# Kernel optimization log

Measured on AMD Instinct MI355X. Metric: run time of the kernel, lower is better.

The kernel has to match this reference:

```python
import jax, jax.numpy as jnp
import numpy as np

B, C, H, W = 8, 512, 64, 64
KD, VD, OD = 64, 512, 512
BN_EPS = 1e-5


def setup_inputs() -> dict:
    key = jax.random.key(0)
    ks = jax.random.split(key, 10)
    s = lambda fan_in: 1.0 / np.sqrt(fan_in)
    return {
        "x": jax.random.normal(ks[0], (B, C, H, W), jnp.float32),
        "Wq": jax.random.normal(ks[1], (KD, C), jnp.float32) * s(C),
        "bq": jnp.zeros((KD,), jnp.float32),
        "Wk": jax.random.normal(ks[2], (KD, C), jnp.float32) * s(C),
        "bk": jnp.zeros((KD,), jnp.float32),
        "Wv": jax.random.normal(ks[3], (VD, C), jnp.float32) * s(C),
        "bv": jnp.zeros((VD,), jnp.float32),
        "gamma": jnp.zeros((1,), jnp.float32),  # torch init: zeros(1)
        "Wf": jax.random.normal(ks[4], (OD, VD), jnp.float32) * s(VD),
        "bn_w": jnp.ones((OD,), jnp.float32),
        "bn_b": jnp.zeros((OD,), jnp.float32),
        "bn_mean": jnp.zeros((OD,), jnp.float32),
        "bn_var": jnp.ones((OD,), jnp.float32),
    }


def reference(x, Wq, bq, Wk, bk, Wv, bv, gamma, Wf, bn_w, bn_b, bn_mean, bn_var):
    b, c, h, w = x.shape
    n = h * w
    # 1x1 convs == per-pixel channel matmuls
    q = jnp.einsum('bchw,kc->bkhw', x, Wq) + bq[None, :, None, None]  # [B,KD,H,W]
    k = jnp.einsum('bchw,kc->bkhw', x, Wk) + bk[None, :, None, None]
    v = jnp.einsum('bchw,vc->bvhw', x, Wv) + bv[None, :, None, None]
    q = q.reshape(b, -1, n)  # [B,KD,N]
    k = k.reshape(b, -1, n)
    v = v.reshape(b, -1, n)  # [B,VD,N]
    # energy[b, i, j] = q[:, :, i] . k[:, :, j]   (proj_query permuted)
    energy = jnp.einsum('bki,bkj->bij', q, k)  # [B,N,N]
    attention = jax.nn.softmax(energy, axis=-1)
    # out = value @ attention^T : out[b, v, i] = sum_j value[b, v, j] * attention[b, i, j]
    out = jnp.einsum('bvj,bij->bvi', v, attention)  # [B,VD,N]
    out = out.reshape(b, c, h, w)
    out = gamma * out + x
    # fuse: 1x1 conv (no bias) -> BatchNorm (inference) -> ReLU
    fused = jnp.einsum('bchw,oc->bohw', out, Wf)
    inv = jax.lax.rsqrt(bn_var + BN_EPS)
    fused = (fused - bn_mean[None, :, None, None]) * (bn_w * inv)[None, :, None, None] + bn_b[None, :, None, None]
    return jax.nn.relu(fused)
```

## Files before the change

### kernel.cpp

```cpp
#include <hip/hip_runtime.h>
#include <hip/hip_bf16.h>

typedef unsigned short u16;
typedef unsigned int u32;
typedef __attribute__((ext_vector_type(8))) short bf16x8;
typedef __attribute__((ext_vector_type(4))) float f32x4;
typedef __attribute__((ext_vector_type(4))) u16 u16x4;

#define B_ 8
#define C_ 512
#define N_ 4096
#define KD_ 64
#define VD_ 512
#define OD_ 512

static __device__ __forceinline__ float bf2f(u16 u) {
    union { u32 i; float f; } z; z.i = ((u32)u) << 16; return z.f;
}
static __device__ __forceinline__ u16 f2bf(float f) {
    union { float f; u32 u; } v; v.f = f;
    u32 r = v.u + 0x7fffu + ((v.u >> 16) & 1u);
    return (u16)(r >> 16);
}
static __device__ __forceinline__ u32 pkbf(float lo, float hi) {
    u32 ul = __float_as_uint(lo) + 0x8000u;
    u32 uh = __float_as_uint(hi) + 0x8000u;
    return __builtin_amdgcn_perm(uh, ul, 0x07060302u);
}
static __device__ __forceinline__ int swz(int row) { return ((row >> 2) + (row >> 4)) & 3; }

static __device__ __forceinline__ void tile_barrier() {
    asm volatile("s_waitcnt lgkmcnt(0)" ::: "memory");
    __builtin_amdgcn_s_barrier();
    asm volatile("" ::: "memory");
}

__global__ __launch_bounds__(256) void transpose_convert_kernel(
    const float* __restrict__ x, const float* __restrict__ Wf,
    const float* __restrict__ gamma,
    u16* __restrict__ xT, u16* __restrict__ Wf16)
{
    const int t = threadIdx.x;
    if (blockIdx.x >= 256) {
        const int tid = (blockIdx.x - 256) * 256 + t;
        const float4* src = (const float4*)Wf + (size_t)tid * 16;
        u16* dst = Wf16 + (size_t)tid * 64;
        #pragma unroll
        for (int j = 0; j < 16; j++) {
            const float4 f = src[j];
            u16x4 p;
            p[0] = f2bf(f.x); p[1] = f2bf(f.y); p[2] = f2bf(f.z); p[3] = f2bf(f.w);
            *(u16x4*)(dst + j * 4) = p;
        }
        return;
    }
    if (gamma[0] == 0.0f) return;
    __shared__ u32 tile[64][33];
    for (int it = 0; it < 16; it++) {
        const int bid = it * 256 + blockIdx.x;
        const int nt = bid & 63;
        const int ct = (bid >> 6) & 7;
        const int b  = bid >> 9;
        const float* xb  = x  + ((size_t)b * C_ + ct * 64) * N_ + nt * 64;
        u16*         xTb = xT + ((size_t)b * N_ + nt * 64) * C_ + ct * 64;
        {
            const int p  = t >> 3;
            const int n8 = t & 7;
            const float* r0 = xb + (size_t)(2 * p)     * N_ + n8 * 8;
            const float* r1 = xb + (size_t)(2 * p + 1) * N_ + n8 * 8;
            const float4 a0 = *(const float4*)(r0);
            const float4 a1 = *(const float4*)(r0 + 4);
            const float4 c0 = *(const float4*)(r1);
            const float4 c1 = *(const float4*)(r1 + 4);
            const float av[8] = { a0.x, a0.y, a0.z, a0.w, a1.x, a1.y, a1.z, a1.w };
            const float cv[8] = { c0.x, c0.y, c0.z, c0.w, c1.x, c1.y, c1.z, c1.w };
            #pragma unroll
            for (int j = 0; j < 8; j++)
                tile[n8 * 8 + j][p] = (u32)f2bf(av[j]) | ((u32)f2bf(cv[j]) << 16);
        }
        __syncthreads();
        #pragma unroll
        for (int h = 0; h < 2; h++) {
            const int id = t + h * 256;
            const int n  = id >> 3;
            const int q  = id & 7;
            uint4 val;
            val.x = tile[n][q * 4 + 0];
            val.y = tile[n][q * 4 + 1];
            val.z = tile[n][q * 4 + 2];
            val.w = tile[n][q * 4 + 3];
            *(uint4*)(xTb + (size_t)n * C_ + q * 8) = val;
        }
        __syncthreads();
    }
}

__global__ __launch_bounds__(256) void proj_kernel(
    const u16* __restrict__ xT,
    const float* __restrict__ Wq, const float* __restrict__ bq,
    const float* __restrict__ Wk, const float* __restrict__ bk,
    const float* __restrict__ Wv, const float* __restrict__ bv,
    const float* __restrict__ gamma,
    u16* __restrict__ q, u16* __restrict__ k, u16* __restrict__ v)
{
    if (gamma[0] == 0.0f) return;
    for (int it = 0; it < 2; it++) {
        const int bid = it * 256 + blockIdx.x;
        const int b = bid >> 6;
        const int p = (bid & 63) * 64 + (threadIdx.x & 63);
        const int dg = threadIdx.x >> 6;
        const u16* xrow = xT + ((size_t)b * N_ + p) * C_;
        for (int d0 = dg * 160; d0 < dg * 160 + 160; d0++) {
            const float* wrow; float bias; u16* dst; int dd; int dim;
            if (d0 < 64)       { dd = d0;       wrow = Wq + (size_t)dd * C_; bias = bq[dd]; dst = q; dim = KD_; }
            else if (d0 < 128) { dd = d0 - 64;  wrow = Wk + (size_t)dd * C_; bias = bk[dd]; dst = k; dim = KD_; }
            else               { dd = d0 - 128; wrow = Wv + (size_t)dd * C_; bias = bv[dd]; dst = v; dim = VD_; }
            float s = bias;
            for (int c = 0; c < C_; c++) s += bf2f(xrow[c]) * wrow[c];
            dst[((size_t)b * dim + dd) * N_ + p] = f2bf(s);
        }
    }
}

__global__ __launch_bounds__(256) void attn_kernel(
    const u16* __restrict__ xT, const u16* __restrict__ q,
    const u16* __restrict__ k, const u16* __restrict__ v,
    const float* __restrict__ gamma, u16* __restrict__ yT)
{
    const float g = gamma[0];
    if (g == 0.0f) return;
    __shared__ float pls[4][64];
    const int wv = threadIdx.x >> 6, lane = threadIdx.x & 63;
    for (int it = 0; it < 4; it++) {
        const int bid = it * 256 + blockIdx.x;
        const int b  = bid >> 7;
        const int q0 = (bid & 127) * 32 + wv * 8;
        const u16* kb = k + (size_t)b * KD_ * N_;
        const u16* vb = v + (size_t)b * VD_ * N_;
        for (int qi = 0; qi < 8; qi++) {
            const int i = q0 + qi;
            const float qv = bf2f(q[((size_t)b * KD_ + lane) * N_ + i]);
            float mx = -1e30f, l = 0.f;
            for (int jb = 0; jb < N_; jb += 64) {
                float e = 0.f;
                for (int kd = 0; kd < 64; kd++)
                    e += __shfl(qv, kd) * bf2f(kb[(size_t)kd * N_ + jb + lane]);
                const float nm = fmaxf(mx, e);
                l = l * __expf(mx - nm) + __expf(e - nm);
                mx = nm;
            }
            for (int off = 32; off; off >>= 1) {
                const float mo = __shfl_xor(mx, off);
                const float lo = __shfl_xor(l, off);
                const float nm = fmaxf(mx, mo);
                l = l * __expf(mx - nm) + lo * __expf(mo - nm);
                mx = nm;
            }
            float oacc[8];
            #pragma unroll
            for (int r = 0; r < 8; r++) oacc[r] = 0.f;
            for (int jb = 0; jb < N_; jb += 64) {
                float e = 0.f;
                for (int kd = 0; kd < 64; kd++)
                    e += __shfl(qv, kd) * bf2f(kb[(size_t)kd * N_ + jb + lane]);
                __syncthreads();
                pls[wv][lane] = __expf(e - mx);
                __syncthreads();
                for (int jj = 0; jj < 64; jj++) {
                    const float p = pls[wv][jj];
                    #pragma unroll
                    for (int r = 0; r < 8; r++)
                        oacc[r] += p * bf2f(vb[(size_t)(r * 64 + lane) * N_ + jb + jj]);
                }
            }
            const float inv = 1.f / l;
            #pragma unroll
            for (int r = 0; r < 8; r++) {
                const size_t idx = ((size_t)b * N_ + i) * C_ + r * 64 + lane;
                yT[idx] = f2bf(g * oacc[r] * inv + bf2f(xT[idx]));
            }
        }
    }
}

__global__ __launch_bounds__(256, 3) void gemm_bn_relu(
    const float* __restrict__ x, const u16* __restrict__ yT,
    const u16* __restrict__ Wf16, const float* __restrict__ gamma,
    const float* __restrict__ bnw, const float* __restrict__ bnb,
    const float* __restrict__ bnm, const float* __restrict__ bnv,
    float* __restrict__ out)
{
    __shared__ u16 lds_x[2][128 * 32];
    __shared__ u16 lds_w[2][128 * 32];

    const int bid = blockIdx.x;
    const int pt8 = bid & 7;
    const int ot  = (bid >> 3) & 3;
    const int g   = bid >> 5;
    const int pt  = (g & 3) * 8 + pt8;
    const int b   = g >> 2;

    const int t = threadIdx.x;
    const int lane = t & 63;
    const int wv = t >> 6;
    const int wm = wv >> 1;
    const int wn = wv & 1;
    const int lcol = lane & 15;
    const int kq = lane >> 4;

    const int rw = t >> 2, posw = t & 3;
    const int ql = (posw - swz(rw)) & 3;
    const u16* WT0 = Wf16 + (size_t)(ot * 128 + rw) * C_ + ql * 8;
    const u16* WT1 = WT0 + (size_t)64 * C_;
    const int wla0 = rw * 32 + posw * 8;
    const int wla1 = wla0 + 64 * 32;

    int aaddr[4], baddr[4];
    #pragma unroll
    for (int i = 0; i < 4; i++) {
        const int P = wm * 64 + i * 16 + lcol;
        aaddr[i] = P * 32 + ((kq + swz(P)) & 3) * 8;
        const int R = wn * 64 + i * 16 + lcol;
        baddr[i] = R * 32 + ((kq + swz(R)) & 3) * 8;
    }

    f32x4 acc[4][4];
    #pragma unroll
    for (int i = 0; i < 4; i++)
        #pragma unroll
        for (int j = 0; j < 4; j++)
            acc[i][j] = (f32x4){0.f, 0.f, 0.f, 0.f};

    auto compute = [&](int buf) {
        bf16x8 af[4], bfg[4];
        #pragma unroll
        for (int mi = 0; mi < 4; mi++)
            af[mi] = *(const bf16x8*)&lds_x[buf][aaddr[mi]];
        #pragma unroll
        for (int ni = 0; ni < 4; ni++)
            bfg[ni] = *(const bf16x8*)&lds_w[buf][baddr[ni]];
        #pragma unroll
        for (int mi = 0; mi < 4; mi++)
            #pragma unroll
            for (int ni = 0; ni < 4; ni++)
                acc[mi][ni] = __builtin_amdgcn_mfma_f32_16x16x32_bf16(
                    af[mi], bfg[ni], acc[mi][ni], 0, 0, 0);
    };

    if (gamma[0] == 0.0f) {
        const int q4 = t & 15, cp = t >> 4;
        int xidx[8];
        #pragma unroll
        for (int j = 0; j < 8; j++) {
            const int p = q4 + 16 * j;
            xidx[j] = p * 16 + (((cp >> 2) + swz(p)) & 3) * 4 + (cp & 3);
        }
        const float* eptr = x + ((size_t)b * C_ + 2 * cp) * N_ + pt * 128 + q4;
        const float* optr = eptr + N_;

        float eA_[8], oA_[8], eB_[8], oB_[8];
        uint4 wA0, wA1, wB0, wB1;
        auto loadA = [&](int ks) {
            const float* ee = eptr + (size_t)ks * 32 * N_;
            const float* oo = optr + (size_t)ks * 32 * N_;
            #pragma unroll
            for (int j = 0; j < 8; j++) { eA_[j] = ee[16 * j]; oA_[j] = oo[16 * j]; }
            wA0 = *(const uint4*)(WT0 + ks * 32);
            wA1 = *(const uint4*)(WT1 + ks * 32);
        };
        auto loadB = [&](int ks) {
            const float* ee = eptr + (size_t)ks * 32 * N_;
            const float* oo = optr + (size_t)ks * 32 * N_;
            #pragma unroll
            for (int j = 0; j < 8; j++) { eB_[j] = ee[16 * j]; oB_[j] = oo[16 * j]; }
            wB0 = *(const uint4*)(WT0 + ks * 32);
            wB1 = *(const uint4*)(WT1 + ks * 32);
        };
        auto writeA = [&](int buf) {
            u32* lx = (u32*)lds_x[buf];
            #pragma unroll
            for (int j = 0; j < 8; j++) lx[xidx[j]] = pkbf(eA_[j], oA_[j]);
            *(uint4*)&lds_w[buf][wla0] = wA0;
            *(uint4*)&lds_w[buf][wla1] = wA1;
        };
        auto writeB = [&](int buf) {
            u32* lx = (u32*)lds_x[buf];
            #pragma unroll
            for (int j = 0; j < 8; j++) lx[xidx[j]] = pkbf(eB_[j], oB_[j]);
            *(uint4*)&lds_w[buf][wla0] = wB0;
            *(uint4*)&lds_w[buf][wla1] = wB1;
        };

        loadA(0); loadB(1);
        writeA(0);
        for (int ks = 0; ks < 16; ks += 2) {
            tile_barrier();
            if (ks + 2 < 16) loadA(ks + 2);
            compute(0);
            writeB(1);
            tile_barrier();
            if (ks + 3 < 16) loadB(ks + 3);
            compute(1);
            if (ks + 2 < 16) writeA(0);
        }
    } else {
        const u16* YT0 = yT + ((size_t)b * N_ + pt * 128 + rw) * C_ + ql * 8;
        const u16* YT1 = YT0 + (size_t)64 * C_;
        uint4 yA0, yA1, yB0, yB1, wA0, wA1, wB0, wB1;
        auto loadA = [&](int ks) {
            yA0 = *(const uint4*)(YT0 + ks * 32);
            yA1 = *(const uint4*)(YT1 + ks * 32);
            wA0 = *(const uint4*)(WT0 + ks * 32);
            wA1 = *(const uint4*)(WT1 + ks * 32);
        };
        auto loadB = [&](int ks) {
            yB0 = *(const uint4*)(YT0 + ks * 32);
            yB1 = *(const uint4*)(YT1 + ks * 32);
            wB0 = *(const uint4*)(WT0 + ks * 32);
            wB1 = *(const uint4*)(WT1 + ks * 32);
        };
        auto writeA = [&](int buf) {
            *(uint4*)&lds_x[buf][wla0] = yA0;
            *(uint4*)&lds_x[buf][wla1] = yA1;
            *(uint4*)&lds_w[buf][wla0] = wA0;
            *(uint4*)&lds_w[buf][wla1] = wA1;
        };
        auto writeB = [&](int buf) {
            *(uint4*)&lds_x[buf][wla0] = yB0;
            *(uint4*)&lds_x[buf][wla1] = yB1;
            *(uint4*)&lds_w[buf][wla0] = wB0;
            *(uint4*)&lds_w[buf][wla1] = wB1;
        };

        loadA(0); loadB(1);
        writeA(0);
        for (int ks = 0; ks < 16; ks += 2) {
            tile_barrier();
            if (ks + 2 < 16) loadA(ks + 2);
            compute(0);
            writeB(1);
            tile_barrier();
            if (ks + 3 < 16) loadB(ks + 3);
            compute(1);
            if (ks + 2 < 16) writeA(0);
        }
    }

    float scale[4], shift[4];
    #pragma unroll
    for (int ni = 0; ni < 4; ni++) {
        const int o = ot * 128 + wn * 64 + ni * 16 + lcol;
        const float s = bnw[o] * rsqrtf(bnv[o] + 1e-5f);
        scale[ni] = s;
        shift[ni] = bnb[o] - bnm[o] * s;
    }
    #pragma unroll
    for (int mi = 0; mi < 4; mi++) {
        const int npix = pt * 128 + wm * 64 + mi * 16 + kq * 4;
        #pragma unroll
        for (int ni = 0; ni < 4; ni++) {
            const int o = ot * 128 + wn * 64 + ni * 16 + lcol;
            f32x4 pk;
            #pragma unroll
            for (int r = 0; r < 4; r++)
                pk[r] = fmaxf(acc[mi][ni][r] * scale[ni] + shift[ni], 0.0f);
            *(f32x4*)(out + ((size_t)b * OD_ + o) * N_ + npix) = pk;
        }
    }
}

extern "C" void kernel_launch(void* const* d_in, const int* in_sizes, int n_in,
                              void* d_out, int out_size, void* d_ws, size_t ws_size,
                              hipStream_t stream) {
    const float* x     = (const float*)d_in[0];
    const float* Wq    = (const float*)d_in[1];
    const float* bq    = (const float*)d_in[2];
    const float* Wk    = (const float*)d_in[3];
    const float* bk    = (const float*)d_in[4];
    const float* Wv    = (const float*)d_in[5];
    const float* bv    = (const float*)d_in[6];
    const float* gamma = (const float*)d_in[7];
    const float* Wf    = (const float*)d_in[8];
    const float* bnw   = (const float*)d_in[9];
    const float* bnb   = (const float*)d_in[10];
    const float* bnm   = (const float*)d_in[11];
    const float* bnv   = (const float*)d_in[12];
    float* out = (float*)d_out;

    char* ws = (char*)d_ws;
    u16* Wf16 = (u16*)(ws);
    u16* xT   = (u16*)(ws + 524288);
    u16* yT   = (u16*)(ws + 34078720);
    u16* q    = (u16*)(ws + 67633152);
    u16* k    = (u16*)(ws + 71827456);
    u16* v    = (u16*)(ws + 76021760);

    transpose_convert_kernel<<<272, 256, 0, stream>>>(x, Wf, gamma, xT, Wf16);
    proj_kernel<<<256, 256, 0, stream>>>(xT, Wq, bq, Wk, bk, Wv, bv, gamma, q, k, v);
    attn_kernel<<<256, 256, 0, stream>>>(xT, q, k, v, gamma, yT);
    gemm_bn_relu<<<1024, 256, 0, stream>>>(x, yT, Wf16, gamma, bnw, bnb, bnm, bnv, out);
}
```

Before: 164.4 us.

## Always transpose x to bf16 and feed GEMM A-operand directly from global

The transpose kernel now always writes xT (bf16, pixel-major), with 1024 blocks each doing 4 tiles, instead of exiting early when gamma is zero. The final GEMM no longer reads fp32 x with strided gathers and LDS packing. It loads A fragments straight from xT/yT into registers with a four-deep register prefetch. Wf is staged in two large LDS halves of 8 k-tiles each, which needs fewer barriers but more LDS and lowers occupancy to 2 blocks per CU. The trade-off is an extra full-tensor transpose pass in exchange for a simpler, more coalesced GEMM.

```diff
diff --git a/kernel.cpp b/kernel.cpp
--- a/kernel.cpp
+++ b/kernel.cpp
@@ -22,11 +22,6 @@
     u32 r = v.u + 0x7fffu + ((v.u >> 16) & 1u);
     return (u16)(r >> 16);
 }
-static __device__ __forceinline__ u32 pkbf(float lo, float hi) {
-    u32 ul = __float_as_uint(lo) + 0x8000u;
-    u32 uh = __float_as_uint(hi) + 0x8000u;
-    return __builtin_amdgcn_perm(uh, ul, 0x07060302u);
-}
 static __device__ __forceinline__ int swz(int row) { return ((row >> 2) + (row >> 4)) & 3; }
 
 static __device__ __forceinline__ void tile_barrier() {
@@ -37,12 +32,11 @@
 
 __global__ __launch_bounds__(256) void transpose_convert_kernel(
     const float* __restrict__ x, const float* __restrict__ Wf,
-    const float* __restrict__ gamma,
     u16* __restrict__ xT, u16* __restrict__ Wf16)
 {
     const int t = threadIdx.x;
-    if (blockIdx.x >= 256) {
-        const int tid = (blockIdx.x - 256) * 256 + t;
+    if (blockIdx.x >= 1024) {
+        const int tid = (blockIdx.x - 1024) * 256 + t;
         const float4* src = (const float4*)Wf + (size_t)tid * 16;
         u16* dst = Wf16 + (size_t)tid * 64;
         #pragma unroll
@@ -54,10 +48,9 @@
         }
         return;
     }
-    if (gamma[0] == 0.0f) return;
     __shared__ u32 tile[64][33];
-    for (int it = 0; it < 16; it++) {
-        const int bid = it * 256 + blockIdx.x;
+    for (int it = 0; it < 4; it++) {
+        const int bid = it * 1024 + blockIdx.x;
         const int nt = bid & 63;
         const int ct = (bid >> 6) & 7;
         const int b  = bid >> 9;
@@ -183,15 +176,14 @@
     }
 }
 
-__global__ __launch_bounds__(256, 3) void gemm_bn_relu(
-    const float* __restrict__ x, const u16* __restrict__ yT,
+__global__ __launch_bounds__(256, 2) void gemm_bn_relu(
+    const u16* __restrict__ xT, const u16* __restrict__ yT,
     const u16* __restrict__ Wf16, const float* __restrict__ gamma,
     const float* __restrict__ bnw, const float* __restrict__ bnb,
     const float* __restrict__ bnm, const float* __restrict__ bnv,
     float* __restrict__ out)
 {
-    __shared__ u16 lds_x[2][128 * 32];
-    __shared__ u16 lds_w[2][128 * 32];
+    __shared__ u16 lds_w[8 * 128 * 32];
 
     const int bid = blockIdx.x;
     const int pt8 = bid & 7;
@@ -215,15 +207,19 @@
     const int wla0 = rw * 32 + posw * 8;
     const int wla1 = wla0 + 64 * 32;
 
-    int aaddr[4], baddr[4];
+    int baddr[4];
     #pragma unroll
     for (int i = 0; i < 4; i++) {
-        const int P = wm * 64 + i * 16 + lcol;
-        aaddr[i] = P * 32 + ((kq + swz(P)) & 3) * 8;
         const int R = wn * 64 + i * 16 + lcol;
         baddr[i] = R * 32 + ((kq + swz(R)) & 3) * 8;
     }
 
+    const u16* Asrc = (gamma[0] == 0.0f) ? xT : yT;
+    const u16* Ab[4];
+    #pragma unroll
+    for (int mi = 0; mi < 4; mi++)
+        Ab[mi] = Asrc + ((size_t)b * N_ + pt * 128 + wm * 64 + mi * 16 + lcol) * C_ + kq * 8;
+
     f32x4 acc[4][4];
     #pragma unroll
     for (int i = 0; i < 4; i++)
@@ -231,14 +227,17 @@
         for (int j = 0; j < 4; j++)
             acc[i][j] = (f32x4){0.f, 0.f, 0.f, 0.f};
 
-    auto compute = [&](int buf) {
-        bf16x8 af[4], bfg[4];
+    auto loadA = [&](bf16x8 (&d)[4], int ks) {
         #pragma unroll
         for (int mi = 0; mi < 4; mi++)
-            af[mi] = *(const bf16x8*)&lds_x[buf][aaddr[mi]];
+            d[mi] = *(const bf16x8*)(Ab[mi] + ks * 32);
+    };
+    auto stepf = [&](bf16x8 (&af)[4], int ks) {
+        const int kt = ks & 7;
+        bf16x8 bfg[4];
         #pragma unroll
         for (int ni = 0; ni < 4; ni++)
-            bfg[ni] = *(const bf16x8*)&lds_w[buf][baddr[ni]];
+            bfg[ni] = *(const bf16x8*)&lds_w[kt * 4096 + baddr[ni]];
         #pragma unroll
         for (int mi = 0; mi < 4; mi++)
             #pragma unroll
@@ -246,105 +245,39 @@
                 acc[mi][ni] = __builtin_amdgcn_mfma_f32_16x16x32_bf16(
                     af[mi], bfg[ni], acc[mi][ni], 0, 0, 0);
     };
-
-    if (gamma[0] == 0.0f) {
-        const int q4 = t & 15, cp = t >> 4;
-        int xidx[8];
-        #pragma unroll
-        for (int j = 0; j < 8; j++) {
-            const int p = q4 + 16 * j;
-            xidx[j] = p * 16 + (((cp >> 2) + swz(p)) & 3) * 4 + (cp & 3);
-        }
-        const float* eptr = x + ((size_t)b * C_ + 2 * cp) * N_ + pt * 128 + q4;
-        const float* optr = eptr + N_;
-
-        float eA_[8], oA_[8], eB_[8], oB_[8];
-        uint4 wA0, wA1, wB0, wB1;
-        auto loadA = [&](int ks) {
-            const float* ee = eptr + (size_t)ks * 32 * N_;
-            const float* oo = optr + (size_t)ks * 32 * N_;
-            #pragma unroll
-            for (int j = 0; j < 8; j++) { eA_[j] = ee[16 * j]; oA_[j] = oo[16 * j]; }
-            wA0 = *(const uint4*)(WT0 + ks * 32);
-            wA1 = *(const uint4*)(WT1 + ks * 32);
-        };
-        auto loadB = [&](int ks) {
-            const float* ee = eptr + (size_t)ks * 32 * N_;
-            const float* oo = optr + (size_t)ks * 32 * N_;
-            #pragma unroll
-            for (int j = 0; j < 8; j++) { eB_[j] = ee[16 * j]; oB_[j] = oo[16 * j]; }
-            wB0 = *(const uint4*)(WT0 + ks * 32);
-            wB1 = *(const uint4*)(WT1 + ks * 32);
-        };
-        auto writeA = [&](int buf) {
-            u32* lx = (u32*)lds_x[buf];
-            #pragma unroll
-            for (int j = 0; j < 8; j++) lx[xidx[j]] = pkbf(eA_[j], oA_[j]);
-            *(uint4*)&lds_w[buf][wla0] = wA0;
-            *(uint4*)&lds_w[buf][wla1] = wA1;
-        };
-        auto writeB = [&](int buf) {
-            u32* lx = (u32*)lds_x[buf];
-            #pragma unroll
-            for (int j = 0; j < 8; j++) lx[xidx[j]] = pkbf(eB_[j], oB_[j]);
-            *(uint4*)&lds_w[buf][wla0] = wB0;
-            *(uint4*)&lds_w[buf][wla1] = wB1;
-        };
-
-        loadA(0); loadB(1);
-        writeA(0);
-        for (int ks = 0; ks < 16; ks += 2) {
-            tile_barrier();
-            if (ks + 2 < 16) loadA(ks + 2);
-            compute(0);
-            writeB(1);
-            tile_barrier();
-            if (ks + 3 < 16) loadB(ks + 3);
-            compute(1);
-            if (ks + 2 < 16) writeA(0);
-        }
-    } else {
-        const u16* YT0 = yT + ((size_t)b * N_ + pt * 128 + rw) * C_ + ql * 8;
-        const u16* YT1 = YT0 + (size_t)64 * C_;
-        uint4 yA0, yA1, yB0, yB1, wA0, wA1, wB0, wB1;
-        auto loadA = [&](int ks) {
-            yA0 = *(const uint4*)(YT0 + ks * 32);
-            yA1 = *(const uint4*)(YT1 + ks * 32);
-            wA0 = *(const uint4*)(WT0 + ks * 32);
-            wA1 = *(const uint4*)(WT1 + ks * 32);
-        };
-        auto loadB = [&](int ks) {
-            yB0 = *(const uint4*)(YT0 + ks * 32);
-            yB1 = *(const uint4*)(YT1 + ks * 32);
-            wB0 = *(const uint4*)(WT0 + ks * 32);
-            wB1 = *(const uint4*)(WT1 + ks * 32);
-        };
-        auto writeA = [&](int buf) {
-            *(uint4*)&lds_x[buf][wla0] = yA0;
-            *(uint4*)&lds_x[buf][wla1] = yA1;
-            *(uint4*)&lds_w[buf][wla0] = wA0;
-            *(uint4*)&lds_w[buf][wla1] = wA1;
-        };
-        auto writeB = [&](int buf) {
-            *(uint4*)&lds_x[buf][wla0] = yB0;
-            *(uint4*)&lds_x[buf][wla1] = yB1;
-            *(uint4*)&lds_w[buf][wla0] = wB0;
-            *(uint4*)&lds_w[buf][wla1] = wB1;
-        };
-
-        loadA(0); loadB(1);
-        writeA(0);
-        for (int ks = 0; ks < 16; ks += 2) {
-            tile_barrier();
-            if (ks + 2 < 16) loadA(ks + 2);
-            compute(0);
-            writeB(1);
-            tile_barrier();
-            if (ks + 3 < 16) loadB(ks + 3);
-            compute(1);
-            if (ks + 2 < 16) writeA(0);
-        }
-    }
+    auto stageW = [&](int half) {
+        #pragma unroll
+        for (int kt = 0; kt < 8; kt++) {
+            const uint4 w0 = *(const uint4*)(WT0 + (half * 8 + kt) * 32);
+            const uint4 w1 = *(const uint4*)(WT1 + (half * 8 + kt) * 32);
+            *(uint4*)&lds_w[kt * 4096 + wla0] = w0;
+            *(uint4*)&lds_w[kt * 4096 + wla1] = w1;
+        }
+    };
+
+    bf16x8 s0[4], s1[4], s2[4], s3[4];
+    loadA(s0, 0); loadA(s1, 1); loadA(s2, 2); loadA(s3, 3);
+    stageW(0);
+    tile_barrier();
+    stepf(s0, 0);  loadA(s0, 4);
+    stepf(s1, 1);  loadA(s1, 5);
+    stepf(s2, 2);  loadA(s2, 6);
+    stepf(s3, 3);  loadA(s3, 7);
+    stepf(s0, 4);  loadA(s0, 8);
+    stepf(s1, 5);  loadA(s1, 9);
+    stepf(s2, 6);  loadA(s2, 10);
+    stepf(s3, 7);  loadA(s3, 11);
+    tile_barrier();
+    stageW(1);
+    tile_barrier();
+    stepf(s0, 8);  loadA(s0, 12);
+    stepf(s1, 9);  loadA(s1, 13);
+    stepf(s2, 10); loadA(s2, 14);
+    stepf(s3, 11); loadA(s3, 15);
+    stepf(s0, 12);
+    stepf(s1, 13);
+    stepf(s2, 14);
+    stepf(s3, 15);
 
     float scale[4], shift[4];
     #pragma unroll
@@ -395,8 +328,8 @@
     u16* k    = (u16*)(ws + 71827456);
     u16* v    = (u16*)(ws + 76021760);
 
-    transpose_convert_kernel<<<272, 256, 0, stream>>>(x, Wf, gamma, xT, Wf16);
+    transpose_convert_kernel<<<1040, 256, 0, stream>>>(x, Wf, xT, Wf16);
     proj_kernel<<<256, 256, 0, stream>>>(xT, Wq, bq, Wk, bk, Wv, bv, gamma, q, k, v);
     attn_kernel<<<256, 256, 0, stream>>>(xT, q, k, v, gamma, yT);
-    gemm_bn_relu<<<1024, 256, 0, stream>>>(x, yT, Wf16, gamma, bnw, bnb, bnm, bnv, out);
-}
+    gemm_bn_relu<<<1024, 256, 0, stream>>>(xT, yT, Wf16, gamma, bnw, bnb, bnm, bnv, out);
+}
```

Result: slower. 179.7 us (+9.3%).
